# Performance work log

Measured on AMD Instinct MI355X. Metric: run time of the kernel, lower is better.

Reference implementation:

```python
import jax, jax.numpy as jnp
import numpy as np

B, C, N = 8, 768, 256
H = 12            # num_heads[0]
D = C // H        # head_dim = 64


def setup_inputs() -> dict:
    key = jax.random.key(0)
    ks = jax.random.split(key, 4)
    s = 0.02
    return {
        "x_ori": jax.random.normal(ks[0], (B, C, N), jnp.float32),
        "cross": jax.random.normal(ks[1], (B, C, N), jnp.float32),
        "W_proj": jax.random.normal(ks[2], (C, C), jnp.float32) * s,
        "b_proj": jnp.zeros((C,), jnp.float32),
        "W_dep": jax.random.normal(ks[3], (C, C), jnp.float32) * s,
        "b_dep": jnp.zeros((C,), jnp.float32),
    }


def reference(x_ori, cross, W_proj, b_proj, W_dep, b_dep):
    # x_ori, cross: [B, C, N] with channel axis factored as (head_dim D, num_heads H)
    Bn, Cn, Nn = x_ori.shape
    Nc = cross.shape[-1]
    scale = D ** (-0.5)

    # 'B (d H) N -> B d (H N)'
    x = x_ori.reshape(Bn, D, H, Nn).reshape(Bn, D, H * Nn)

    # proj over channel axis (1x1 conv): [B, C, Nc]
    cp = jnp.einsum('oc,bcn->bon', W_proj, cross) + b_proj[None, :, None]
    cp = cp.reshape(Bn, D, H, Nc).reshape(Bn, D, H * Nc)      # 'B (d H) Nc -> B d (H Nc)'

    # 'B (d H) Nc -> B (H Nc) d'
    cr = cross.reshape(Bn, D, H, Nc).transpose(0, 2, 3, 1).reshape(Bn, H * Nc, D)

    # raw attention (no softmax in original source)
    atten = jnp.einsum('bdm,bdn->bmn', x, cp) * scale          # [B, H*N, H*Nc]
    out = jnp.einsum('bmn,bnd->bmd', atten, cr)                # [B, H*N, D]

    # 'B (N H) d -> B N (H d)'  (note (num, head) grouping per source)
    out = out.reshape(Bn, Nn, H, D).reshape(Bn, Nn, H * D)

    y = out @ W_dep.T + b_dep                                  # deproj: [B, N, C]
    # skip connection (dropout is identity at eval / drop_ratio=0)
    return x_ori + y.transpose(0, 2, 1)
```

## Files before the change

kernel.cpp:

```cpp
#include <hip/hip_runtime.h>

typedef unsigned short u16;
typedef short bf16x8 __attribute__((ext_vector_type(8)));
typedef float f32x4 __attribute__((ext_vector_type(4)));

#define BB 8
#define CC 768
#define NN 256
#define HH 12
#define DD 64
#define K3 3072
#define BCN 196608
#define SCALE 0.125f
#define LDP 72

__device__ __forceinline__ u16 f2b(float f) {
    union { float f; unsigned int i; } v; v.f = f;
    unsigned int r = v.i + 0x7FFFu + ((v.i >> 16) & 1u);
    return (u16)(r >> 16);
}

__global__ __launch_bounds__(256) void k_proj(
    const float* __restrict__ Wp, const float* __restrict__ cross,
    const float* __restrict__ bp, u16* __restrict__ cp, float* __restrict__ G)
{
    __shared__ __align__(16) u16 As[64 * LDP];
    __shared__ __align__(16) u16 Bs[64 * LDP];
    __shared__ __align__(16) float T[64][68];
    const int n0 = blockIdx.x * 64;
    const int o0 = blockIdx.y * 64;
    const int b  = blockIdx.z;
    const int t = threadIdx.x;
    const int lane = t & 63, wave = t >> 6;
    const int q = lane >> 4, tx = lane & 15;
    const int wm = (wave & 1) * 32, wn = (wave >> 1) * 32;

    if (blockIdx.x == 0 && blockIdx.y == 0) {
        float4 z = {0.f, 0.f, 0.f, 0.f};
        float* Gb = G + b * 4096;
        #pragma unroll
        for (int j = 0; j < 4; ++j)
            *reinterpret_cast<float4*>(Gb + t * 4 + j * 1024) = z;
    }

    const float* crb = cross + b * BCN;
    f32x4 acc[2][2] = {};
    for (int c0 = 0; c0 < CC; c0 += 64) {
        {
            const int r = t >> 2, cq = t & 3;
            const float* src = Wp + (o0 + r) * CC + c0;
            u16* dst = As + r * LDP;
            #pragma unroll
            for (int u = 0; u < 4; ++u) {
                const int cl = (cq + 4 * u) * 4;
                float4 v = *reinterpret_cast<const float4*>(src + cl);
                ushort4 w; w.x = f2b(v.x); w.y = f2b(v.y); w.z = f2b(v.z); w.w = f2b(v.w);
                *reinterpret_cast<ushort4*>(dst + cl) = w;
            }
        }
        {
            const int r = t >> 2, fq = t & 3;
            const float* src = crb + (c0 + r) * NN + n0;
            #pragma unroll
            for (int u = 0; u < 4; ++u) {
                const int nl = (fq + 4 * u) * 4;
                float4 v = *reinterpret_cast<const float4*>(src + nl);
                T[r][nl + 0] = v.x; T[r][nl + 1] = v.y; T[r][nl + 2] = v.z; T[r][nl + 3] = v.w;
            }
        }
        __syncthreads();
        {
            const int nn = t >> 2, cq = t & 3;
            u16* dst = Bs + nn * LDP;
            #pragma unroll
            for (int u = 0; u < 4; ++u) {
                const int c4 = (cq + 4 * u) * 4;
                ushort4 w;
                w.x = f2b(T[c4 + 0][nn]); w.y = f2b(T[c4 + 1][nn]);
                w.z = f2b(T[c4 + 2][nn]); w.w = f2b(T[c4 + 3][nn]);
                *reinterpret_cast<ushort4*>(dst + c4) = w;
            }
        }
        __syncthreads();
        #pragma unroll
        for (int kk = 0; kk < 2; ++kk) {
            bf16x8 a0 = *reinterpret_cast<bf16x8*>(As + (wm + tx) * LDP + kk * 32 + q * 8);
            bf16x8 a1 = *reinterpret_cast<bf16x8*>(As + (wm + 16 + tx) * LDP + kk * 32 + q * 8);
            bf16x8 b0 = *reinterpret_cast<bf16x8*>(Bs + (wn + tx) * LDP + kk * 32 + q * 8);
            bf16x8 b1 = *reinterpret_cast<bf16x8*>(Bs + (wn + 16 + tx) * LDP + kk * 32 + q * 8);
            acc[0][0] = __builtin_amdgcn_mfma_f32_16x16x32_bf16(a0, b0, acc[0][0], 0, 0, 0);
            acc[0][1] = __builtin_amdgcn_mfma_f32_16x16x32_bf16(a0, b1, acc[0][1], 0, 0, 0);
            acc[1][0] = __builtin_amdgcn_mfma_f32_16x16x32_bf16(a1, b0, acc[1][0], 0, 0, 0);
            acc[1][1] = __builtin_amdgcn_mfma_f32_16x16x32_bf16(a1, b1, acc[1][1], 0, 0, 0);
        }
        __syncthreads();
    }
    u16* cpb = cp + b * BCN;
    #pragma unroll
    for (int i = 0; i < 2; ++i)
        #pragma unroll
        for (int j = 0; j < 2; ++j)
            #pragma unroll
            for (int r = 0; r < 4; ++r) {
                const int o = o0 + wm + i * 16 + q * 4 + r;
                const int n = n0 + wn + j * 16 + tx;
                cpb[o * NN + n] = f2b(acc[i][j][r] + bp[o]);
            }
}

__global__ __launch_bounds__(256) void k_gram(
    const float* __restrict__ cross, const u16* __restrict__ cp, float* __restrict__ G)
{
    __shared__ __align__(16) u16 As[64 * LDP];
    __shared__ __align__(16) u16 Bs[64 * LDP];
    const int kb = blockIdx.x * 64;
    const int b  = blockIdx.y;
    const int t = threadIdx.x;
    const int lane = t & 63, wave = t >> 6;
    const int q = lane >> 4, tx = lane & 15;
    const int wm = (wave & 1) * 32, wn = (wave >> 1) * 32;
    const float* crb = cross + b * BCN;
    const u16* cpb = cp + b * BCN;
    f32x4 acc[2][2] = {};
    {
        const int r = t >> 2, cq = t & 3;
        const float* src = crb + r * K3 + kb;
        u16* dst = As + r * LDP;
        #pragma unroll
        for (int u = 0; u < 4; ++u) {
            const int cl = (cq + 4 * u) * 4;
            float4 v = *reinterpret_cast<const float4*>(src + cl);
            ushort4 w; w.x = f2b(v.x); w.y = f2b(v.y); w.z = f2b(v.z); w.w = f2b(v.w);
            *reinterpret_cast<ushort4*>(dst + cl) = w;
        }
    }
    {
        const int r = t >> 3, ch = (t & 7) * 8;
        *reinterpret_cast<uint4*>(Bs + r * LDP + ch) =
            *reinterpret_cast<const uint4*>(cpb + r * K3 + kb + ch);
        *reinterpret_cast<uint4*>(Bs + (r + 32) * LDP + ch) =
            *reinterpret_cast<const uint4*>(cpb + (r + 32) * K3 + kb + ch);
    }
    __syncthreads();
    #pragma unroll
    for (int kk = 0; kk < 2; ++kk) {
        bf16x8 a0 = *reinterpret_cast<bf16x8*>(As + (wm + tx) * LDP + kk * 32 + q * 8);
        bf16x8 a1 = *reinterpret_cast<bf16x8*>(As + (wm + 16 + tx) * LDP + kk * 32 + q * 8);
        bf16x8 b0 = *reinterpret_cast<bf16x8*>(Bs + (wn + tx) * LDP + kk * 32 + q * 8);
        bf16x8 b1 = *reinterpret_cast<bf16x8*>(Bs + (wn + 16 + tx) * LDP + kk * 32 + q * 8);
        acc[0][0] = __builtin_amdgcn_mfma_f32_16x16x32_bf16(a0, b0, acc[0][0], 0, 0, 0);
        acc[0][1] = __builtin_amdgcn_mfma_f32_16x16x32_bf16(a0, b1, acc[0][1], 0, 0, 0);
        acc[1][0] = __builtin_amdgcn_mfma_f32_16x16x32_bf16(a1, b0, acc[1][0], 0, 0, 0);
        acc[1][1] = __builtin_amdgcn_mfma_f32_16x16x32_bf16(a1, b1, acc[1][1], 0, 0, 0);
    }
    float* Gb = G + b * 4096;
    #pragma unroll
    for (int i = 0; i < 2; ++i)
        #pragma unroll
        for (int j = 0; j < 2; ++j)
            #pragma unroll
            for (int r = 0; r < 4; ++r) {
                const int dd = wm + i * 16 + q * 4 + r;
                const int d  = wn + j * 16 + tx;
                atomicAdd(Gb + dd * DD + d, acc[i][j][r] * SCALE);
            }
}

__global__ __launch_bounds__(256) void k_xm(
    const float* __restrict__ x, const float* __restrict__ G, u16* __restrict__ U)
{
    __shared__ __align__(16) u16 As[64 * LDP];
    __shared__ __align__(16) u16 Bs[64 * LDP];
    __shared__ __align__(16) float T[64][68];
    const int m0 = blockIdx.x * 64;
    const int b  = blockIdx.y;
    const int h   = m0 >> 8;
    const int nn0 = m0 & 255;
    const int t = threadIdx.x;
    const int lane = t & 63, wave = t >> 6;
    const int q = lane >> 4, tx = lane & 15;
    const int wm = (wave & 1) * 32, wn = (wave >> 1) * 32;
    const float* xb = x + b * BCN;
    const float* Gb = G + b * 4096;
    f32x4 acc[2][2] = {};
    {
        const int d = t >> 2, fq = t & 3;
        const float* src = xb + (d * HH + h) * NN + nn0;
        #pragma unroll
        for (int u = 0; u < 4; ++u) {
            const int nl = (fq + 4 * u) * 4;
            float4 v = *reinterpret_cast<const float4*>(src + nl);
            T[d][nl + 0] = v.x; T[d][nl + 1] = v.y; T[d][nl + 2] = v.z; T[d][nl + 3] = v.w;
        }
    }
    {
        const int r = t >> 2, cq = t & 3;
        const float* src = Gb + r * DD;
        u16* dst = Bs + r * LDP;
        #pragma unroll
        for (int u = 0; u < 4; ++u) {
            const int cl = (cq + 4 * u) * 4;
            float4 v = *reinterpret_cast<const float4*>(src + cl);
            ushort4 w; w.x = f2b(v.x); w.y = f2b(v.y); w.z = f2b(v.z); w.w = f2b(v.w);
            *reinterpret_cast<ushort4*>(dst + cl) = w;
        }
    }
    __syncthreads();
    {
        const int nn = t >> 2, dq = t & 3;
        u16* dst = As + nn * LDP;
        #pragma unroll
        for (int u = 0; u < 4; ++u) {
            const int d4 = (dq + 4 * u) * 4;
            ushort4 w;
            w.x = f2b(T[d4 + 0][nn]); w.y = f2b(T[d4 + 1][nn]);
            w.z = f2b(T[d4 + 2][nn]); w.w = f2b(T[d4 + 3][nn]);
            *reinterpret_cast<ushort4*>(dst + d4) = w;
        }
    }
    __syncthreads();
    #pragma unroll
    for (int kk = 0; kk < 2; ++kk) {
        bf16x8 a0 = *reinterpret_cast<bf16x8*>(As + (wm + tx) * LDP + kk * 32 + q * 8);
        bf16x8 a1 = *reinterpret_cast<bf16x8*>(As + (wm + 16 + tx) * LDP + kk * 32 + q * 8);
        bf16x8 b0 = *reinterpret_cast<bf16x8*>(Bs + (wn + tx) * LDP + kk * 32 + q * 8);
        bf16x8 b1 = *reinterpret_cast<bf16x8*>(Bs + (wn + 16 + tx) * LDP + kk * 32 + q * 8);
        acc[0][0] = __builtin_amdgcn_mfma_f32_16x16x32_bf16(a0, b0, acc[0][0], 0, 0, 0);
        acc[0][1] = __builtin_amdgcn_mfma_f32_16x16x32_bf16(a0, b1, acc[0][1], 0, 0, 0);
        acc[1][0] = __builtin_amdgcn_mfma_f32_16x16x32_bf16(a1, b0, acc[1][0], 0, 0, 0);
        acc[1][1] = __builtin_amdgcn_mfma_f32_16x16x32_bf16(a1, b1, acc[1][1], 0, 0, 0);
    }
    u16* Ub = U + b * BCN;
    #pragma unroll
    for (int i = 0; i < 2; ++i)
        #pragma unroll
        for (int j = 0; j < 2; ++j)
            #pragma unroll
            for (int r = 0; r < 4; ++r) {
                const int m  = m0 + wm + i * 16 + q * 4 + r;
                const int dd = wn + j * 16 + tx;
                Ub[m * DD + dd] = f2b(acc[i][j][r]);
            }
}

__global__ __launch_bounds__(256) void k_dep(
    const float* __restrict__ Wd, const u16* __restrict__ U,
    const float* __restrict__ bd, const float* __restrict__ x, float* __restrict__ out)
{
    __shared__ __align__(16) u16 As[64 * LDP];
    __shared__ __align__(16) u16 Bs[64 * LDP];
    const int n0 = blockIdx.x * 64;
    const int o0 = blockIdx.y * 64;
    const int b  = blockIdx.z;
    const int t = threadIdx.x;
    const int lane = t & 63, wave = t >> 6;
    const int q = lane >> 4, tx = lane & 15;
    const int wm = (wave & 1) * 32, wn = (wave >> 1) * 32;
    const u16* Ub = U + b * BCN;
    f32x4 acc[2][2] = {};
    for (int c0 = 0; c0 < CC; c0 += 64) {
        {
            const int r = t >> 2, cq = t & 3;
            const float* src = Wd + (o0 + r) * CC + c0;
            u16* dst = As + r * LDP;
            #pragma unroll
            for (int u = 0; u < 4; ++u) {
                const int cl = (cq + 4 * u) * 4;
                float4 v = *reinterpret_cast<const float4*>(src + cl);
                ushort4 w; w.x = f2b(v.x); w.y = f2b(v.y); w.z = f2b(v.z); w.w = f2b(v.w);
                *reinterpret_cast<ushort4*>(dst + cl) = w;
            }
        }
        {
            const int r = t >> 3, ch = (t & 7) * 8;
            *reinterpret_cast<uint4*>(Bs + r * LDP + ch) =
                *reinterpret_cast<const uint4*>(Ub + (n0 + r) * CC + c0 + ch);
            *reinterpret_cast<uint4*>(Bs + (r + 32) * LDP + ch) =
                *reinterpret_cast<const uint4*>(Ub + (n0 + r + 32) * CC + c0 + ch);
        }
        __syncthreads();
        #pragma unroll
        for (int kk = 0; kk < 2; ++kk) {
            bf16x8 a0 = *reinterpret_cast<bf16x8*>(As + (wm + tx) * LDP + kk * 32 + q * 8);
            bf16x8 a1 = *reinterpret_cast<bf16x8*>(As + (wm + 16 + tx) * LDP + kk * 32 + q * 8);
            bf16x8 b0 = *reinterpret_cast<bf16x8*>(Bs + (wn + tx) * LDP + kk * 32 + q * 8);
            bf16x8 b1 = *reinterpret_cast<bf16x8*>(Bs + (wn + 16 + tx) * LDP + kk * 32 + q * 8);
            acc[0][0] = __builtin_amdgcn_mfma_f32_16x16x32_bf16(a0, b0, acc[0][0], 0, 0, 0);
            acc[0][1] = __builtin_amdgcn_mfma_f32_16x16x32_bf16(a0, b1, acc[0][1], 0, 0, 0);
            acc[1][0] = __builtin_amdgcn_mfma_f32_16x16x32_bf16(a1, b0, acc[1][0], 0, 0, 0);
            acc[1][1] = __builtin_amdgcn_mfma_f32_16x16x32_bf16(a1, b1, acc[1][1], 0, 0, 0);
        }
        __syncthreads();
    }
    #pragma unroll
    for (int i = 0; i < 2; ++i)
        #pragma unroll
        for (int j = 0; j < 2; ++j)
            #pragma unroll
            for (int r = 0; r < 4; ++r) {
                const int o = o0 + wm + i * 16 + q * 4 + r;
                const int n = n0 + wn + j * 16 + tx;
                const int idx = b * BCN + o * NN + n;
                out[idx] = acc[i][j][r] + bd[o] + x[idx];
            }
}

extern "C" void kernel_launch(void* const* d_in, const int* in_sizes, int n_in,
                              void* d_out, int out_size, void* d_ws, size_t ws_size,
                              hipStream_t stream) {
    const float* x_ori = (const float*)d_in[0];
    const float* cross = (const float*)d_in[1];
    const float* Wp    = (const float*)d_in[2];
    const float* bp    = (const float*)d_in[3];
    const float* Wd    = (const float*)d_in[4];
    const float* bd    = (const float*)d_in[5];
    float* out = (float*)d_out;

    u16*   cp = (u16*)d_ws;
    u16*   U  = (u16*)d_ws;
    float* G  = (float*)((char*)d_ws + (size_t)BB * BCN * sizeof(u16));

    k_proj<<<dim3(4, 12, BB), 256, 0, stream>>>(Wp, cross, bp, cp, G);
    k_gram<<<dim3(48, BB), 256, 0, stream>>>(cross, cp, G);
    k_xm  <<<dim3(48, BB), 256, 0, stream>>>(x_ori, G, U);
    k_dep <<<dim3(4, 12, BB), 256, 0, stream>>>(Wd, U, bd, x_ori, out);
}
```

Baseline: 123.7 us.

## Fuse projection and gram kernels, register-prefetch loads, double-buffer deproj

Merges the projection GEMM and the gram (cross^T·cp) reduction into one kernel. Each block computes a head-strided 64x64 tile of the projected cross and immediately multiplies it with the matching cross tile, so the bf16 cp intermediate is never written to or read from global memory. The projection loop prefetches the next k-slice into registers, and the deproj GEMM gets double-buffered LDS with register prefetch and one barrier per iteration. G zeroing moves to a hipMemsetAsync. This drops a kernel launch and a round trip through global memory, at the cost of an extra memset op and more register pressure.

```diff
diff --git a/kernel.cpp b/kernel.cpp
--- a/kernel.cpp
+++ b/kernel.cpp
@@ -9,7 +9,6 @@
 #define NN 256
 #define HH 12
 #define DD 64
-#define K3 3072
 #define BCN 196608
 #define SCALE 0.125f
 #define LDP 72
@@ -20,61 +19,75 @@
     return (u16)(r >> 16);
 }
 
-__global__ __launch_bounds__(256) void k_proj(
+#define MFMA8(ASP, BSP, ACC)                                                              \
+    _Pragma("unroll")                                                                     \
+    for (int kk = 0; kk < 2; ++kk) {                                                      \
+        bf16x8 a0 = *reinterpret_cast<bf16x8*>((ASP) + (wm + tx) * LDP + kk * 32 + q * 8);\
+        bf16x8 a1 = *reinterpret_cast<bf16x8*>((ASP) + (wm + 16 + tx) * LDP + kk * 32 + q * 8);\
+        bf16x8 b0 = *reinterpret_cast<bf16x8*>((BSP) + (wn + tx) * LDP + kk * 32 + q * 8);\
+        bf16x8 b1 = *reinterpret_cast<bf16x8*>((BSP) + (wn + 16 + tx) * LDP + kk * 32 + q * 8);\
+        ACC[0][0] = __builtin_amdgcn_mfma_f32_16x16x32_bf16(a0, b0, ACC[0][0], 0, 0, 0);  \
+        ACC[0][1] = __builtin_amdgcn_mfma_f32_16x16x32_bf16(a0, b1, ACC[0][1], 0, 0, 0);  \
+        ACC[1][0] = __builtin_amdgcn_mfma_f32_16x16x32_bf16(a1, b0, ACC[1][0], 0, 0, 0);  \
+        ACC[1][1] = __builtin_amdgcn_mfma_f32_16x16x32_bf16(a1, b1, ACC[1][1], 0, 0, 0);  \
+    }
+
+__global__ __launch_bounds__(256) void k_pg(
     const float* __restrict__ Wp, const float* __restrict__ cross,
-    const float* __restrict__ bp, u16* __restrict__ cp, float* __restrict__ G)
+    const float* __restrict__ bp, float* __restrict__ G)
 {
     __shared__ __align__(16) u16 As[64 * LDP];
     __shared__ __align__(16) u16 Bs[64 * LDP];
     __shared__ __align__(16) float T[64][68];
-    const int n0 = blockIdx.x * 64;
-    const int o0 = blockIdx.y * 64;
+    const int h  = blockIdx.x;
+    const int n0 = blockIdx.y * 64;
     const int b  = blockIdx.z;
     const int t = threadIdx.x;
     const int lane = t & 63, wave = t >> 6;
     const int q = lane >> 4, tx = lane & 15;
     const int wm = (wave & 1) * 32, wn = (wave >> 1) * 32;
-
-    if (blockIdx.x == 0 && blockIdx.y == 0) {
-        float4 z = {0.f, 0.f, 0.f, 0.f};
-        float* Gb = G + b * 4096;
-        #pragma unroll
-        for (int j = 0; j < 4; ++j)
-            *reinterpret_cast<float4*>(Gb + t * 4 + j * 1024) = z;
-    }
-
+    const int r4 = t >> 2, cq = t & 3;
     const float* crb = cross + b * BCN;
+    const float* wrow = Wp + (r4 * HH + h) * CC;
+
     f32x4 acc[2][2] = {};
-    for (int c0 = 0; c0 < CC; c0 += 64) {
+    float4 ra[4], rc[4];
+    #pragma unroll
+    for (int u = 0; u < 4; ++u) {
+        const int cl = (cq + 4 * u) * 4;
+        ra[u] = *reinterpret_cast<const float4*>(wrow + cl);
+        rc[u] = *reinterpret_cast<const float4*>(crb + r4 * NN + n0 + cl);
+    }
+    for (int it = 0; it < 12; ++it) {
+        if (it > 0) __syncthreads();
         {
-            const int r = t >> 2, cq = t & 3;
-            const float* src = Wp + (o0 + r) * CC + c0;
-            u16* dst = As + r * LDP;
+            u16* dstA = As + r4 * LDP;
             #pragma unroll
             for (int u = 0; u < 4; ++u) {
                 const int cl = (cq + 4 * u) * 4;
-                float4 v = *reinterpret_cast<const float4*>(src + cl);
-                ushort4 w; w.x = f2b(v.x); w.y = f2b(v.y); w.z = f2b(v.z); w.w = f2b(v.w);
-                *reinterpret_cast<ushort4*>(dst + cl) = w;
-            }
-        }
-        {
-            const int r = t >> 2, fq = t & 3;
-            const float* src = crb + (c0 + r) * NN + n0;
+                ushort4 w; w.x = f2b(ra[u].x); w.y = f2b(ra[u].y);
+                w.z = f2b(ra[u].z); w.w = f2b(ra[u].w);
+                *reinterpret_cast<ushort4*>(dstA + cl) = w;
+                T[r4][cl + 0] = rc[u].x; T[r4][cl + 1] = rc[u].y;
+                T[r4][cl + 2] = rc[u].z; T[r4][cl + 3] = rc[u].w;
+            }
+        }
+        if (it < 11) {
+            const int c0 = (it + 1) * 64;
             #pragma unroll
             for (int u = 0; u < 4; ++u) {
-                const int nl = (fq + 4 * u) * 4;
-                float4 v = *reinterpret_cast<const float4*>(src + nl);
-                T[r][nl + 0] = v.x; T[r][nl + 1] = v.y; T[r][nl + 2] = v.z; T[r][nl + 3] = v.w;
+                const int cl = (cq + 4 * u) * 4;
+                ra[u] = *reinterpret_cast<const float4*>(wrow + c0 + cl);
+                rc[u] = *reinterpret_cast<const float4*>(crb + (c0 + r4) * NN + n0 + cl);
             }
         }
         __syncthreads();
         {
-            const int nn = t >> 2, cq = t & 3;
+            const int nn = t >> 2, dq = t & 3;
             u16* dst = Bs + nn * LDP;
             #pragma unroll
             for (int u = 0; u < 4; ++u) {
-                const int c4 = (cq + 4 * u) * 4;
+                const int c4 = (dq + 4 * u) * 4;
                 ushort4 w;
                 w.x = f2b(T[c4 + 0][nn]); w.y = f2b(T[c4 + 1][nn]);
                 w.z = f2b(T[c4 + 2][nn]); w.w = f2b(T[c4 + 3][nn]);
@@ -82,77 +95,36 @@
             }
         }
         __syncthreads();
-        #pragma unroll
-        for (int kk = 0; kk < 2; ++kk) {
-            bf16x8 a0 = *reinterpret_cast<bf16x8*>(As + (wm + tx) * LDP + kk * 32 + q * 8);
-            bf16x8 a1 = *reinterpret_cast<bf16x8*>(As + (wm + 16 + tx) * LDP + kk * 32 + q * 8);
-            bf16x8 b0 = *reinterpret_cast<bf16x8*>(Bs + (wn + tx) * LDP + kk * 32 + q * 8);
-            bf16x8 b1 = *reinterpret_cast<bf16x8*>(Bs + (wn + 16 + tx) * LDP + kk * 32 + q * 8);
-            acc[0][0] = __builtin_amdgcn_mfma_f32_16x16x32_bf16(a0, b0, acc[0][0], 0, 0, 0);
-            acc[0][1] = __builtin_amdgcn_mfma_f32_16x16x32_bf16(a0, b1, acc[0][1], 0, 0, 0);
-            acc[1][0] = __builtin_amdgcn_mfma_f32_16x16x32_bf16(a1, b0, acc[1][0], 0, 0, 0);
-            acc[1][1] = __builtin_amdgcn_mfma_f32_16x16x32_bf16(a1, b1, acc[1][1], 0, 0, 0);
-        }
-        __syncthreads();
-    }
-    u16* cpb = cp + b * BCN;
-    #pragma unroll
-    for (int i = 0; i < 2; ++i)
-        #pragma unroll
-        for (int j = 0; j < 2; ++j)
-            #pragma unroll
-            for (int r = 0; r < 4; ++r) {
-                const int o = o0 + wm + i * 16 + q * 4 + r;
-                const int n = n0 + wn + j * 16 + tx;
-                cpb[o * NN + n] = f2b(acc[i][j][r] + bp[o]);
-            }
-}
-
-__global__ __launch_bounds__(256) void k_gram(
-    const float* __restrict__ cross, const u16* __restrict__ cp, float* __restrict__ G)
-{
-    __shared__ __align__(16) u16 As[64 * LDP];
-    __shared__ __align__(16) u16 Bs[64 * LDP];
-    const int kb = blockIdx.x * 64;
-    const int b  = blockIdx.y;
-    const int t = threadIdx.x;
-    const int lane = t & 63, wave = t >> 6;
-    const int q = lane >> 4, tx = lane & 15;
-    const int wm = (wave & 1) * 32, wn = (wave >> 1) * 32;
-    const float* crb = cross + b * BCN;
-    const u16* cpb = cp + b * BCN;
-    f32x4 acc[2][2] = {};
-    {
-        const int r = t >> 2, cq = t & 3;
-        const float* src = crb + r * K3 + kb;
-        u16* dst = As + r * LDP;
+        MFMA8(As, Bs, acc)
+    }
+    __syncthreads();
+    float4 rg[4];
+    #pragma unroll
+    for (int u = 0; u < 4; ++u)
+        rg[u] = *reinterpret_cast<const float4*>(crb + (r4 * HH + h) * NN + n0 + (cq + 4 * u) * 4);
+    #pragma unroll
+    for (int i = 0; i < 2; ++i)
+        #pragma unroll
+        for (int r = 0; r < 4; ++r) {
+            const int ddl = wm + i * 16 + q * 4 + r;
+            const float bias = bp[ddl * HH + h];
+            #pragma unroll
+            for (int j = 0; j < 2; ++j)
+                As[ddl * LDP + wn + j * 16 + tx] = f2b(acc[i][j][r] + bias);
+        }
+    {
+        u16* dst = Bs + r4 * LDP;
         #pragma unroll
         for (int u = 0; u < 4; ++u) {
             const int cl = (cq + 4 * u) * 4;
-            float4 v = *reinterpret_cast<const float4*>(src + cl);
-            ushort4 w; w.x = f2b(v.x); w.y = f2b(v.y); w.z = f2b(v.z); w.w = f2b(v.w);
+            ushort4 w; w.x = f2b(rg[u].x); w.y = f2b(rg[u].y);
+            w.z = f2b(rg[u].z); w.w = f2b(rg[u].w);
             *reinterpret_cast<ushort4*>(dst + cl) = w;
         }
     }
-    {
-        const int r = t >> 3, ch = (t & 7) * 8;
-        *reinterpret_cast<uint4*>(Bs + r * LDP + ch) =
-            *reinterpret_cast<const uint4*>(cpb + r * K3 + kb + ch);
-        *reinterpret_cast<uint4*>(Bs + (r + 32) * LDP + ch) =
-            *reinterpret_cast<const uint4*>(cpb + (r + 32) * K3 + kb + ch);
-    }
-    __syncthreads();
-    #pragma unroll
-    for (int kk = 0; kk < 2; ++kk) {
-        bf16x8 a0 = *reinterpret_cast<bf16x8*>(As + (wm + tx) * LDP + kk * 32 + q * 8);
-        bf16x8 a1 = *reinterpret_cast<bf16x8*>(As + (wm + 16 + tx) * LDP + kk * 32 + q * 8);
-        bf16x8 b0 = *reinterpret_cast<bf16x8*>(Bs + (wn + tx) * LDP + kk * 32 + q * 8);
-        bf16x8 b1 = *reinterpret_cast<bf16x8*>(Bs + (wn + 16 + tx) * LDP + kk * 32 + q * 8);
-        acc[0][0] = __builtin_amdgcn_mfma_f32_16x16x32_bf16(a0, b0, acc[0][0], 0, 0, 0);
-        acc[0][1] = __builtin_amdgcn_mfma_f32_16x16x32_bf16(a0, b1, acc[0][1], 0, 0, 0);
-        acc[1][0] = __builtin_amdgcn_mfma_f32_16x16x32_bf16(a1, b0, acc[1][0], 0, 0, 0);
-        acc[1][1] = __builtin_amdgcn_mfma_f32_16x16x32_bf16(a1, b1, acc[1][1], 0, 0, 0);
-    }
+    __syncthreads();
+    f32x4 g[2][2] = {};
+    MFMA8(As, Bs, g)
     float* Gb = G + b * 4096;
     #pragma unroll
     for (int i = 0; i < 2; ++i)
@@ -161,8 +133,8 @@
             #pragma unroll
             for (int r = 0; r < 4; ++r) {
                 const int dd = wm + i * 16 + q * 4 + r;
-                const int d  = wn + j * 16 + tx;
-                atomicAdd(Gb + dd * DD + d, acc[i][j][r] * SCALE);
+                const int dc = wn + j * 16 + tx;
+                atomicAdd(Gb + dc * DD + dd, g[i][j][r] * SCALE);
             }
 }
 
@@ -219,17 +191,7 @@
         }
     }
     __syncthreads();
-    #pragma unroll
-    for (int kk = 0; kk < 2; ++kk) {
-        bf16x8 a0 = *reinterpret_cast<bf16x8*>(As + (wm + tx) * LDP + kk * 32 + q * 8);
-        bf16x8 a1 = *reinterpret_cast<bf16x8*>(As + (wm + 16 + tx) * LDP + kk * 32 + q * 8);
-        bf16x8 b0 = *reinterpret_cast<bf16x8*>(Bs + (wn + tx) * LDP + kk * 32 + q * 8);
-        bf16x8 b1 = *reinterpret_cast<bf16x8*>(Bs + (wn + 16 + tx) * LDP + kk * 32 + q * 8);
-        acc[0][0] = __builtin_amdgcn_mfma_f32_16x16x32_bf16(a0, b0, acc[0][0], 0, 0, 0);
-        acc[0][1] = __builtin_amdgcn_mfma_f32_16x16x32_bf16(a0, b1, acc[0][1], 0, 0, 0);
-        acc[1][0] = __builtin_amdgcn_mfma_f32_16x16x32_bf16(a1, b0, acc[1][0], 0, 0, 0);
-        acc[1][1] = __builtin_amdgcn_mfma_f32_16x16x32_bf16(a1, b1, acc[1][1], 0, 0, 0);
-    }
+    MFMA8(As, Bs, acc)
     u16* Ub = U + b * BCN;
     #pragma unroll
     for (int i = 0; i < 2; ++i)
@@ -247,8 +209,8 @@
     const float* __restrict__ Wd, const u16* __restrict__ U,
     const float* __restrict__ bd, const float* __restrict__ x, float* __restrict__ out)
 {
-    __shared__ __align__(16) u16 As[64 * LDP];
-    __shared__ __align__(16) u16 Bs[64 * LDP];
+    __shared__ __align__(16) u16 As[2][64 * LDP];
+    __shared__ __align__(16) u16 Bs[2][64 * LDP];
     const int n0 = blockIdx.x * 64;
     const int o0 = blockIdx.y * 64;
     const int b  = blockIdx.z;
@@ -256,41 +218,43 @@
     const int lane = t & 63, wave = t >> 6;
     const int q = lane >> 4, tx = lane & 15;
     const int wm = (wave & 1) * 32, wn = (wave >> 1) * 32;
+    const int r4 = t >> 2, cq = t & 3;
+    const int r8 = t >> 3, ch = (t & 7) * 8;
     const u16* Ub = U + b * BCN;
+    float4 ra[4]; uint4 rb[2];
+
+    auto loadit = [&](int it) {
+        const int c0 = it * 64;
+        const float* srcA = Wd + (o0 + r4) * CC + c0;
+        #pragma unroll
+        for (int u = 0; u < 4; ++u)
+            ra[u] = *reinterpret_cast<const float4*>(srcA + (cq + 4 * u) * 4);
+        rb[0] = *reinterpret_cast<const uint4*>(Ub + (n0 + r8) * CC + c0 + ch);
+        rb[1] = *reinterpret_cast<const uint4*>(Ub + (n0 + r8 + 32) * CC + c0 + ch);
+    };
+    auto storeit = [&](int buf) {
+        u16* dst = As[buf] + r4 * LDP;
+        #pragma unroll
+        for (int u = 0; u < 4; ++u) {
+            const int cl = (cq + 4 * u) * 4;
+            ushort4 w; w.x = f2b(ra[u].x); w.y = f2b(ra[u].y);
+            w.z = f2b(ra[u].z); w.w = f2b(ra[u].w);
+            *reinterpret_cast<ushort4*>(dst + cl) = w;
+        }
+        *reinterpret_cast<uint4*>(Bs[buf] + r8 * LDP + ch) = rb[0];
+        *reinterpret_cast<uint4*>(Bs[buf] + (r8 + 32) * LDP + ch) = rb[1];
+    };
+
     f32x4 acc[2][2] = {};
-    for (int c0 = 0; c0 < CC; c0 += 64) {
-        {
-            const int r = t >> 2, cq = t & 3;
-            const float* src = Wd + (o0 + r) * CC + c0;
-            u16* dst = As + r * LDP;
-            #pragma unroll
-            for (int u = 0; u < 4; ++u) {
-                const int cl = (cq + 4 * u) * 4;
-                float4 v = *reinterpret_cast<const float4*>(src + cl);
-                ushort4 w; w.x = f2b(v.x); w.y = f2b(v.y); w.z = f2b(v.z); w.w = f2b(v.w);
-                *reinterpret_cast<ushort4*>(dst + cl) = w;
-            }
-        }
-        {
-            const int r = t >> 3, ch = (t & 7) * 8;
-            *reinterpret_cast<uint4*>(Bs + r * LDP + ch) =
-                *reinterpret_cast<const uint4*>(Ub + (n0 + r) * CC + c0 + ch);
-            *reinterpret_cast<uint4*>(Bs + (r + 32) * LDP + ch) =
-                *reinterpret_cast<const uint4*>(Ub + (n0 + r + 32) * CC + c0 + ch);
-        }
+    loadit(0);
+    storeit(0);
+    #pragma unroll 2
+    for (int it = 0; it < 12; ++it) {
+        const int cur = it & 1;
+        if (it < 11) loadit(it + 1);
         __syncthreads();
-        #pragma unroll
-        for (int kk = 0; kk < 2; ++kk) {
-            bf16x8 a0 = *reinterpret_cast<bf16x8*>(As + (wm + tx) * LDP + kk * 32 + q * 8);
-            bf16x8 a1 = *reinterpret_cast<bf16x8*>(As + (wm + 16 + tx) * LDP + kk * 32 + q * 8);
-            bf16x8 b0 = *reinterpret_cast<bf16x8*>(Bs + (wn + tx) * LDP + kk * 32 + q * 8);
-            bf16x8 b1 = *reinterpret_cast<bf16x8*>(Bs + (wn + 16 + tx) * LDP + kk * 32 + q * 8);
-            acc[0][0] = __builtin_amdgcn_mfma_f32_16x16x32_bf16(a0, b0, acc[0][0], 0, 0, 0);
-            acc[0][1] = __builtin_amdgcn_mfma_f32_16x16x32_bf16(a0, b1, acc[0][1], 0, 0, 0);
-            acc[1][0] = __builtin_amdgcn_mfma_f32_16x16x32_bf16(a1, b0, acc[1][0], 0, 0, 0);
-            acc[1][1] = __builtin_amdgcn_mfma_f32_16x16x32_bf16(a1, b1, acc[1][1], 0, 0, 0);
-        }
-        __syncthreads();
+        MFMA8(As[cur], Bs[cur], acc)
+        if (it < 11) storeit(cur ^ 1);
     }
     #pragma unroll
     for (int i = 0; i < 2; ++i)
@@ -316,12 +280,11 @@
     const float* bd    = (const float*)d_in[5];
     float* out = (float*)d_out;
 
-    u16*   cp = (u16*)d_ws;
     u16*   U  = (u16*)d_ws;
     float* G  = (float*)((char*)d_ws + (size_t)BB * BCN * sizeof(u16));
 
-    k_proj<<<dim3(4, 12, BB), 256, 0, stream>>>(Wp, cross, bp, cp, G);
-    k_gram<<<dim3(48, BB), 256, 0, stream>>>(cross, cp, G);
-    k_xm  <<<dim3(48, BB), 256, 0, stream>>>(x_ori, G, U);
-    k_dep <<<dim3(4, 12, BB), 256, 0, stream>>>(Wd, U, bd, x_ori, out);
-}
+    hipMemsetAsync(G, 0, (size_t)BB * DD * DD * sizeof(float), stream);
+    k_pg <<<dim3(HH, 4, BB), 256, 0, stream>>>(Wp, cross, bp, G);
+    k_xm <<<dim3(48, BB), 256, 0, stream>>>(x_ori, G, U);
+    k_dep<<<dim3(4, 12, BB), 256, 0, stream>>>(Wd, U, bd, x_ori, out);
+}
```

New measurement: 133.3 us. 1.08x slower.
